# Kernel optimization log

Measured on AMD Instinct MI355X. Metric: run time of the kernel, lower is better.

## Reference

```python
import jax, jax.numpy as jnp
import numpy as np

B, LQ, LK, D, H, DK, DV = 8, 1024, 1024, 512, 8, 64, 64
EPS = 1e-14          # K.epsilon()**2 with default K.epsilon()=1e-7
MASK_VALUE = -1e30   # default mask_value in call()


def setup_inputs() -> dict:
    key = jax.random.key(0)
    ks = jax.random.split(key, 7)
    query = jax.random.normal(ks[0], (B, LQ, D), jnp.float32)
    key_t = jax.random.normal(ks[1], (B, LK, D), jnp.float32)
    value = jax.random.normal(ks[2], (B, LK, D), jnp.float32)
    mask = jax.random.randint(ks[3], (B, LK), 0, 2).astype(jnp.float32)
    glorot = np.sqrt(2.0 / (D + DK)).astype(np.float32)
    Wq = jax.random.normal(ks[4], (H, D, DK), jnp.float32) * glorot
    Wk = jax.random.normal(ks[5], (H, D, DK), jnp.float32) * glorot
    Wv = jax.random.normal(ks[6], (H, D, DV), jnp.float32) * glorot
    gamma = jnp.ones((1,), jnp.float32)
    beta = jnp.zeros((1,), jnp.float32)
    return {"query": query, "key": key_t, "value": value, "mask": mask,
            "Wq": Wq, "Wk": Wk, "Wv": Wv, "gamma": gamma, "beta": beta}


def reference(query, key, value, mask, Wq, Wk, Wv, gamma, beta):
    # Per-head projections (the original's Python loop over heads, vectorized).
    q = jnp.einsum('bqd,hde->bhqe', query, Wq)   # [B,H,LQ,DK]
    k = jnp.einsum('bkd,hde->bhke', key, Wk)     # [B,H,LK,DK]
    v = jnp.einsum('bkd,hde->bhke', value, Wv)   # [B,H,LK,DV]
    # NOTE: no 1/sqrt(dk) scaling, faithful to the source.
    A = jnp.einsum('bhqe,bhke->bhqk', q, k)      # [B,H,LQ,LK]
    m = mask[:, None, None, :]                    # [B,1,1,LK] broadcast over heads & queries
    A = m * A + (1.0 - m) * MASK_VALUE
    A = jax.nn.softmax(A, axis=-1)
    o = jnp.einsum('bhqk,bhke->bhqe', A, v)      # [B,H,LQ,DV]
    conc = o.transpose(0, 2, 1, 3).reshape(B, LQ, H * DV)  # concat heads
    # Scalar-affine layernorm over the concatenated feature dim.
    mean = jnp.mean(conc, axis=-1, keepdims=True)
    var = jnp.mean(jnp.square(conc - mean), axis=-1, keepdims=True)
    x = (conc - mean) / jnp.sqrt(var + EPS)
    return x * gamma[0] + beta[0]
```

## Files before the change

### kernel.cpp

```cpp
#include <hip/hip_runtime.h>
#include <math.h>

#define NB 8
#define NLQ 1024
#define NLK 1024
#define ND 512
#define NH 8
#define MASKV -1e30f
#define LOG2E 1.44269504088896f
#define SHIFT2 32.0f

typedef unsigned short ushort_t;
typedef __attribute__((ext_vector_type(8))) _Float16 f16x8;
typedef __attribute__((ext_vector_type(8))) short bf16x8;
typedef __attribute__((ext_vector_type(16))) float f32x16;

__device__ __forceinline__ ushort_t f2h_bits(float f) {
    union { _Float16 h; ushort_t u; } v; v.h = (_Float16)f;
    return v.u;
}
__device__ __forceinline__ ushort_t f2bf(float f) {
    union { float f; unsigned u; } v; v.f = f;
    unsigned r = v.u + 0x7fffu + ((v.u >> 16) & 1u);
    return (ushort_t)(r >> 16);
}
__device__ __forceinline__ void gload16(const ushort_t* g, ushort_t* l) {
    __builtin_amdgcn_global_load_lds(
        (const __attribute__((address_space(1))) void*)g,
        (__attribute__((address_space(3))) void*)l, 16, 0, 0);
}
__device__ __forceinline__ unsigned pack_bf16_trunc(float p0, float p1) {
    return __builtin_amdgcn_perm(__float_as_uint(p1), __float_as_uint(p0),
                                 0x07060302u);
}

__global__ __launch_bounds__(256) void wsplit_kernel(
    const float* __restrict__ Wq, const float* __restrict__ Wk, const float* __restrict__ Wv,
    ushort_t* __restrict__ oq, ushort_t* __restrict__ ok, ushort_t* __restrict__ ov) {
    __shared__ float T[64][65];
    const int d0 = blockIdx.x * 64;
    const int h  = blockIdx.y;
    const int t  = blockIdx.z;
    const float* W = (t == 0) ? Wq : (t == 1) ? Wk : Wv;
    ushort_t* oh = (t == 0) ? oq : (t == 1) ? ok : ov;
    const int tid = threadIdx.x;
#pragma unroll
    for (int i = 0; i < 4; i++) {
        int r = (tid >> 4) + i * 16;
        int c = (tid & 15) * 4;
        float4 v = *(const float4*)&W[((size_t)h * ND + d0 + r) * 64 + c];
        *(float4*)&T[r][c] = v;
    }
    __syncthreads();
    const int e = tid & 63;
    const int dg = tid >> 6;
    ushort_t hs[16];
#pragma unroll
    for (int dd = 0; dd < 16; dd++) hs[dd] = f2h_bits(T[dg * 16 + dd][e]);
    size_t base = ((size_t)h * 64 + e) * ND + d0 + dg * 16;
#pragma unroll
    for (int c = 0; c < 2; c++) {
        uint4 wh;
        wh.x = (unsigned)hs[8*c+0] | ((unsigned)hs[8*c+1] << 16);
        wh.y = (unsigned)hs[8*c+2] | ((unsigned)hs[8*c+3] << 16);
        wh.z = (unsigned)hs[8*c+4] | ((unsigned)hs[8*c+5] << 16);
        wh.w = (unsigned)hs[8*c+6] | ((unsigned)hs[8*c+7] << 16);
        *(uint4*)&oh[base + 8 * c] = wh;
    }
}

__global__ __launch_bounds__(256, 2) void proj_gemm_kernel(
    const float* __restrict__ Xq, const float* __restrict__ Xk,
    const float* __restrict__ Xv, const ushort_t* __restrict__ Wbase,
    ushort_t* __restrict__ Obase) {
    __shared__ ushort_t sA[2][8320];
    __shared__ ushort_t sB[2][8320];

    const int bid   = blockIdx.x;
    const int y     = bid / 192;
    const int mglob = bid % 192;
    const int t  = mglob >> 6;
    const int b  = (mglob >> 3) & 7;
    const int l0 = (mglob & 7) * 128;

    const int tid  = threadIdx.x;
    const int wave = tid >> 6;
    const int lane = tid & 63;
    const int l31  = lane & 31;
    const int hib  = lane >> 5;
    const int wr = wave >> 1, wc = wave & 1;

    const float* Xt = (t == 0) ? Xq : (t == 1) ? Xk : Xv;
    const float* gx = Xt + ((size_t)b * NLQ + l0) * ND;
    const ushort_t* gwt = Wbase + (size_t)t * ((size_t)NH * 64 * ND)
                        + (size_t)y * 128 * ND;
    ushort_t* out = Obase + (size_t)t * ((size_t)NB * NH * NLQ * 64);

    const int srow = lane >> 3;
    const int schk = (lane & 7) ^ srow;

    float4 ax[4][2];
    auto aload = [&](int d0) {
#pragma unroll
        for (int j = 0; j < 4; j++) {
            int row = (j * 4 + wave) * 8 + srow;
            const float* p = gx + (size_t)row * ND + d0 + schk * 8;
            ax[j][0] = *(const float4*)p;
            ax[j][1] = *(const float4*)(p + 4);
        }
    };
    auto awrite = [&](int buf) {
#pragma unroll
        for (int j = 0; j < 4; j++) {
            int u = j * 4 + wave;
            uint4 hv;
            hv.x = (unsigned)f2h_bits(ax[j][0].x) | ((unsigned)f2h_bits(ax[j][0].y) << 16);
            hv.y = (unsigned)f2h_bits(ax[j][0].z) | ((unsigned)f2h_bits(ax[j][0].w) << 16);
            hv.z = (unsigned)f2h_bits(ax[j][1].x) | ((unsigned)f2h_bits(ax[j][1].y) << 16);
            hv.w = (unsigned)f2h_bits(ax[j][1].z) | ((unsigned)f2h_bits(ax[j][1].w) << 16);
            *(uint4*)(sA[buf] + u * 520 + lane * 8) = hv;
        }
    };
    auto bstage = [&](int buf, int d0) {
#pragma unroll
        for (int j = 0; j < 4; j++) {
            int u = j * 4 + wave;
            int row = u * 8 + srow;
            gload16(gwt + (size_t)row * ND + d0 + schk * 8, sB[buf] + u * 520);
        }
    };

    f32x16 acc00, acc01, acc10, acc11;
#pragma unroll
    for (int i = 0; i < 16; i++) { acc00[i] = 0.f; acc01[i] = 0.f;
                                   acc10[i] = 0.f; acc11[i] = 0.f; }

    const int ga  = wr * 8 + (l31 >> 3);
    const int gb  = wc * 8 + (l31 >> 3);
    const int ro  = (l31 & 7) * 64;
    const int swz = l31 & 7;

    auto mfma_chunk = [&](int buf) {
#pragma unroll
        for (int c = 0; c < 4; c++) {
            const int pc = ((2 * c + hib) ^ swz) * 8;
            f16x8 a0 = *(const f16x8*)&sA[buf][ga * 520 + ro + pc];
            f16x8 a1 = *(const f16x8*)&sA[buf][(ga + 4) * 520 + ro + pc];
            f16x8 b0 = *(const f16x8*)&sB[buf][gb * 520 + ro + pc];
            f16x8 b1 = *(const f16x8*)&sB[buf][(gb + 4) * 520 + ro + pc];
            acc00 = __builtin_amdgcn_mfma_f32_32x32x16_f16(a0, b0, acc00, 0, 0, 0);
            acc01 = __builtin_amdgcn_mfma_f32_32x32x16_f16(a0, b1, acc01, 0, 0, 0);
            acc10 = __builtin_amdgcn_mfma_f32_32x32x16_f16(a1, b0, acc10, 0, 0, 0);
            acc11 = __builtin_amdgcn_mfma_f32_32x32x16_f16(a1, b1, acc11, 0, 0, 0);
        }
    };

    aload(0);
    bstage(0, 0);
    asm volatile("s_waitcnt vmcnt(4)" ::: "memory");
    __builtin_amdgcn_sched_barrier(0);
    awrite(0);
    aload(64);
    asm volatile("s_waitcnt vmcnt(8)" ::: "memory");
    asm volatile("s_waitcnt lgkmcnt(0)" ::: "memory");
    __builtin_amdgcn_sched_barrier(0);
    __builtin_amdgcn_s_barrier();

    int cur = 0;
#pragma unroll
    for (int kc = 0; kc < 8; kc++) {
        if (kc < 7) {
            bstage(cur ^ 1, (kc + 1) * 64);
            mfma_chunk(cur);
            asm volatile("s_waitcnt vmcnt(4)" ::: "memory");
            __builtin_amdgcn_sched_barrier(0);
            awrite(cur ^ 1);
            if (kc < 6) {
                aload((kc + 2) * 64);
                asm volatile("s_waitcnt vmcnt(8)" ::: "memory");
            } else {
                asm volatile("s_waitcnt vmcnt(0)" ::: "memory");
            }
            asm volatile("s_waitcnt lgkmcnt(0)" ::: "memory");
            __builtin_amdgcn_sched_barrier(0);
            __builtin_amdgcn_s_barrier();
        } else {
            mfma_chunk(cur);
        }
        cur ^= 1;
    }

    if (t < 2) {
        const float scale = (t == 0) ? LOG2E : 1.f;
#pragma unroll
        for (int mi = 0; mi < 2; mi++) {
#pragma unroll
            for (int ni = 0; ni < 2; ni++) {
                const f32x16& a = (mi == 0) ? (ni == 0 ? acc00 : acc01)
                                            : (ni == 0 ? acc10 : acc11);
                int nglob = y * 128 + wc * 64 + ni * 32 + l31;
                int hh = nglob >> 6, e = nglob & 63;
                size_t obase = (((size_t)b * NH + hh) * NLQ + l0) * 64 + e;
#pragma unroll
                for (int r = 0; r < 16; r++) {
                    int l = wr * 64 + mi * 32 + (r & 3) + 8 * (r >> 2) + 4 * hib;
                    out[obase + (size_t)l * 64] = f2h_bits(a[r] * scale);
                }
            }
        }
    } else {
        __syncthreads();
        ushort_t (*T)[130] = (ushort_t(*)[130])sA;
#pragma unroll
        for (int mi = 0; mi < 2; mi++) {
#pragma unroll
            for (int ni = 0; ni < 2; ni++) {
                const f32x16& a = (mi == 0) ? (ni == 0 ? acc00 : acc01)
                                            : (ni == 0 ? acc10 : acc11);
                int n_loc = wc * 64 + ni * 32 + l31;
#pragma unroll
                for (int r = 0; r < 16; r++) {
                    int l = wr * 64 + mi * 32 + (r & 3) + 8 * (r >> 2) + 4 * hib;
                    T[n_loc][l] = f2bf(a[r]);
                }
            }
        }
        __syncthreads();
        const int n_loc = tid >> 1;
        const int half  = tid & 1;
        const int hh = n_loc >> 6, e = n_loc & 63;
        size_t obase = (((size_t)b * NH + y * 2 + hh) * 64 + e) * NLK
                     + l0 + half * 64;
        const ushort_t* src = &T[n_loc][half * 64];
#pragma unroll
        for (int c2 = 0; c2 < 8; c2++)
            *(uint4*)&out[obase + c2 * 8] = *(const uint4*)&src[c2 * 8];
    }
}

__global__ __launch_bounds__(256, 4) void attn_kernel(
    const ushort_t* __restrict__ Qf, const ushort_t* __restrict__ Kf,
    const ushort_t* __restrict__ Vt, const float* __restrict__ maskp,
    float* __restrict__ Op) {
    __shared__ ushort_t sK[2][4160];
    __shared__ ushort_t sV[2][4160];
    __shared__ float sBias[1024];

    const int idx = blockIdx.x;
    const int bh_i = idx & 63;
    const int qc  = idx >> 6;
    const int b = bh_i >> 3, h = bh_i & 7;
    const size_t bh = (size_t)b * NH + h;

    const int tid  = threadIdx.x;
    const int wave = tid >> 6;
    const int lane = tid & 63;
    const int l31  = lane & 31;
    const int hib  = lane >> 5;
    const int q = qc * 128 + wave * 32 + l31;
    const int sw = l31 & 7;

    {
        const float* mrow = maskp + ((size_t)b << 10);
        float4 m0 = *(const float4*)&mrow[tid * 4];
        float4 bi;
        bi.x = (m0.x > 0.5f) ? -SHIFT2 : MASKV;
        bi.y = (m0.y > 0.5f) ? -SHIFT2 : MASKV;
        bi.z = (m0.z > 0.5f) ? -SHIFT2 : MASKV;
        bi.w = (m0.w > 0.5f) ? -SHIFT2 : MASKV;
        *(float4*)&sBias[tid * 4] = bi;
    }

    f16x8 qh[4];
    {
        const ushort_t* ph = Qf + (bh * NLQ + q) * 64 + hib * 8;
#pragma unroll
        for (int c = 0; c < 4; c++) qh[c] = *(const f16x8*)(ph + c * 16);
    }

    const int srow = lane >> 3;
    const int schk = (lane & 7) ^ srow;

    auto stage = [&](int buf, int k0) {
#pragma unroll
        for (int n = 0; n < 4; n++) {
            int u = wave + n * 4;
            if (u < 8) {
                int row = u * 8 + srow;
                int key = (row & ~12) | ((row & 4) << 1) | ((row & 8) >> 1);
                gload16(Kf + ((bh << 10) + k0 + key) * 64 + schk * 8,
                        sK[buf] + u * 520);
            } else {
                int u8 = u - 8;
                int row = u8 * 8 + srow;
                gload16(Vt + ((bh << 6) + row) * NLK + k0 + schk * 8,
                        sV[buf] + u8 * 520);
            }
        }
    };

    f32x16 O0, O1;
#pragma unroll
    for (int i = 0; i < 16; i++) { O0[i] = 0.f; O1[i] = 0.f; }
    float lrun = 0.f;

    const int rp0 = (l31 >> 3) * 520 + (l31 & 7) * 64;
    const int rp1 = rp0 + 4 * 520;

    stage(0, 0);
    __syncthreads();
    int cur = 0;

    for (int t = 0; t < 16; t++) {
        const int k0 = t << 6;
        if (t < 15) stage(cur ^ 1, k0 + 64);

        f32x16 S0, S1;
#pragma unroll
        for (int g = 0; g < 4; g++) {
            const int kb = k0 + 16 * (g >> 1) + 8 * hib + 4 * (g & 1);
            float4 b0 = *(const float4*)&sBias[kb];
            float4 b1 = *(const float4*)&sBias[kb + 32];
            S0[4 * g + 0] = b0.x; S0[4 * g + 1] = b0.y;
            S0[4 * g + 2] = b0.z; S0[4 * g + 3] = b0.w;
            S1[4 * g + 0] = b1.x; S1[4 * g + 1] = b1.y;
            S1[4 * g + 2] = b1.z; S1[4 * g + 3] = b1.w;
        }
#pragma unroll
        for (int c = 0; c < 4; c++) {
            const int pc = ((2 * c + hib) ^ sw) * 8;
            f16x8 a0 = *(const f16x8*)&sK[cur][rp0 + pc];
            f16x8 a1 = *(const f16x8*)&sK[cur][rp1 + pc];
            S0 = __builtin_amdgcn_mfma_f32_32x32x16_f16(a0, qh[c], S0, 0, 0, 0);
            S1 = __builtin_amdgcn_mfma_f32_32x32x16_f16(a1, qh[c], S1, 0, 0, 0);
        }

        unsigned pq[8][2];
#pragma unroll
        for (int g = 0; g < 8; g++) {
            float p0, p1, p2, p3;
            if (g < 4) {
                p0 = __builtin_amdgcn_exp2f(S0[4*g+0]);
                p1 = __builtin_amdgcn_exp2f(S0[4*g+1]);
                p2 = __builtin_amdgcn_exp2f(S0[4*g+2]);
                p3 = __builtin_amdgcn_exp2f(S0[4*g+3]);
            } else {
                p0 = __builtin_amdgcn_exp2f(S1[4*(g-4)+0]);
                p1 = __builtin_amdgcn_exp2f(S1[4*(g-4)+1]);
                p2 = __builtin_amdgcn_exp2f(S1[4*(g-4)+2]);
                p3 = __builtin_amdgcn_exp2f(S1[4*(g-4)+3]);
            }
            lrun += (p0 + p1) + (p2 + p3);
            pq[g][0] = pack_bf16_trunc(p0, p1);
            pq[g][1] = pack_bf16_trunc(p2, p3);
        }

#pragma unroll
        for (int c = 0; c < 4; c++) {
            union { unsigned u[4]; bf16x8 v; } pf;
            pf.u[0] = pq[2 * c][0];     pf.u[1] = pq[2 * c][1];
            pf.u[2] = pq[2 * c + 1][0]; pf.u[3] = pq[2 * c + 1][1];
            const int pc = ((2 * c + hib) ^ sw) * 8;
            bf16x8 v0 = *(const bf16x8*)&sV[cur][rp0 + pc];
            bf16x8 v1 = *(const bf16x8*)&sV[cur][rp1 + pc];
            O0 = __builtin_amdgcn_mfma_f32_32x32x16_bf16(v0, pf.v, O0, 0, 0, 0);
            O1 = __builtin_amdgcn_mfma_f32_32x32x16_bf16(v1, pf.v, O1, 0, 0, 0);
        }
        __syncthreads();
        cur ^= 1;
    }

    lrun += __shfl_xor(lrun, 32);
    const float linv = 1.f / lrun;
    float* obase = Op + ((size_t)(b * NLQ + q)) * (NH * 64) + h * 64;
#pragma unroll
    for (int me = 0; me < 2; me++) {
#pragma unroll
        for (int g = 0; g < 4; g++) {
            int e0 = me * 32 + 8 * g + 4 * hib;
            float4 o;
            if (me == 0) {
                o.x = O0[4 * g + 0] * linv; o.y = O0[4 * g + 1] * linv;
                o.z = O0[4 * g + 2] * linv; o.w = O0[4 * g + 3] * linv;
            } else {
                o.x = O1[4 * g + 0] * linv; o.y = O1[4 * g + 1] * linv;
                o.z = O1[4 * g + 2] * linv; o.w = O1[4 * g + 3] * linv;
            }
            *(float4*)&obase[e0] = o;
        }
    }
}

__global__ __launch_bounds__(256) void ln_kernel(const float* __restrict__ X,
                                                 const float* __restrict__ gamma,
                                                 const float* __restrict__ beta,
                                                 float* __restrict__ out) {
    const int row = blockIdx.x * 4 + (threadIdx.x >> 6);
    const int lane = threadIdx.x & 63;
    const float* x = &X[(size_t)row * 512];
    float4 v0 = *(const float4*)&x[lane * 8];
    float4 v1 = *(const float4*)&x[lane * 8 + 4];
    float sum = v0.x + v0.y + v0.z + v0.w + v1.x + v1.y + v1.z + v1.w;
    float sq = v0.x * v0.x + v0.y * v0.y + v0.z * v0.z + v0.w * v0.w
             + v1.x * v1.x + v1.y * v1.y + v1.z * v1.z + v1.w * v1.w;
#pragma unroll
    for (int off = 32; off > 0; off >>= 1) {
        sum += __shfl_down(sum, off);
        sq  += __shfl_down(sq, off);
    }
    sum = __shfl(sum, 0);
    sq  = __shfl(sq, 0);
    const float mean = sum * (1.f / 512.f);
    const float var = sq * (1.f / 512.f) - mean * mean;
    const float rstd = rsqrtf(var + 1e-14f);
    const float g = gamma[0], be = beta[0];
    float* o = &out[(size_t)row * 512];
    float4 r0, r1;
    r0.x = (v0.x - mean) * rstd * g + be;  r0.y = (v0.y - mean) * rstd * g + be;
    r0.z = (v0.z - mean) * rstd * g + be;  r0.w = (v0.w - mean) * rstd * g + be;
    r1.x = (v1.x - mean) * rstd * g + be;  r1.y = (v1.y - mean) * rstd * g + be;
    r1.z = (v1.z - mean) * rstd * g + be;  r1.w = (v1.w - mean) * rstd * g + be;
    *(float4*)&o[lane * 8] = r0;
    *(float4*)&o[lane * 8 + 4] = r1;
}

extern "C" void kernel_launch(void* const* d_in, const int* in_sizes, int n_in,
                              void* d_out, int out_size, void* d_ws, size_t ws_size,
                              hipStream_t stream) {
    const float* query = (const float*)d_in[0];
    const float* key_t = (const float*)d_in[1];
    const float* value = (const float*)d_in[2];
    const float* mask  = (const float*)d_in[3];
    const float* Wq    = (const float*)d_in[4];
    const float* Wk    = (const float*)d_in[5];
    const float* Wv    = (const float*)d_in[6];
    const float* gamma = (const float*)d_in[7];
    const float* beta  = (const float*)d_in[8];
    float* out = (float*)d_out;

    const size_t A = (size_t)NB * NLQ * ND;
    const size_t WS = (size_t)NH * 64 * ND;
    ushort_t* Qf = (ushort_t*)d_ws;
    ushort_t* Kf = Qf + A;
    ushort_t* Vt = Qf + 2 * A;
    ushort_t* Wt = Qf + 3 * A;

    wsplit_kernel<<<dim3(ND / 64, NH, 3), 256, 0, stream>>>(
        Wq, Wk, Wv, Wt, Wt + WS, Wt + 2 * WS);

    proj_gemm_kernel<<<768, 256, 0, stream>>>(
        query, key_t, value, Wt, Qf);

    attn_kernel<<<512, 256, 0, stream>>>(Qf, Kf, Vt, mask, out);

    ln_kernel<<<(NB * NLQ) / 4, 256, 0, stream>>>(out, gamma, beta, out);
}
```

Measured before the change: 165.4 us.

## Load projection weight fragments directly from global memory instead of via LDS

```diff
diff --git a/kernel.cpp b/kernel.cpp
--- a/kernel.cpp
+++ b/kernel.cpp
@@ -69,12 +69,11 @@
     }
 }
 
-__global__ __launch_bounds__(256, 2) void proj_gemm_kernel(
+__global__ __launch_bounds__(256, 3) void proj_gemm_kernel(
     const float* __restrict__ Xq, const float* __restrict__ Xk,
     const float* __restrict__ Xv, const ushort_t* __restrict__ Wbase,
     ushort_t* __restrict__ Obase) {
     __shared__ ushort_t sA[2][8320];
-    __shared__ ushort_t sB[2][8320];
 
     const int bid   = blockIdx.x;
     const int y     = bid / 192;
@@ -121,14 +120,6 @@
             *(uint4*)(sA[buf] + u * 520 + lane * 8) = hv;
         }
     };
-    auto bstage = [&](int buf, int d0) {
-#pragma unroll
-        for (int j = 0; j < 4; j++) {
-            int u = j * 4 + wave;
-            int row = u * 8 + srow;
-            gload16(gwt + (size_t)row * ND + d0 + schk * 8, sB[buf] + u * 520);
-        }
-    };
 
     f32x16 acc00, acc01, acc10, acc11;
 #pragma unroll
@@ -136,57 +127,39 @@
                                    acc10[i] = 0.f; acc11[i] = 0.f; }
 
     const int ga  = wr * 8 + (l31 >> 3);
-    const int gb  = wc * 8 + (l31 >> 3);
     const int ro  = (l31 & 7) * 64;
     const int swz = l31 & 7;
 
-    auto mfma_chunk = [&](int buf) {
+    const ushort_t* gb0 = gwt
+        + (size_t)(wc * 64 + (l31 >> 3) * 8 + (l31 & 7)) * ND;
+
+    aload(0);
+    awrite(0);
+    __syncthreads();
+
+    int cur = 0;
+#pragma unroll
+    for (int kc = 0; kc < 8; kc++) {
+        if (kc < 7) aload((kc + 1) * 64);
+        f16x8 bfr[2][4];
+#pragma unroll
+        for (int ni = 0; ni < 2; ni++)
+#pragma unroll
+            for (int c = 0; c < 4; c++)
+                bfr[ni][c] = *(const f16x8*)&gb0[(size_t)ni * 32 * ND
+                                                 + kc * 64 + (2 * c + hib) * 8];
 #pragma unroll
         for (int c = 0; c < 4; c++) {
             const int pc = ((2 * c + hib) ^ swz) * 8;
-            f16x8 a0 = *(const f16x8*)&sA[buf][ga * 520 + ro + pc];
-            f16x8 a1 = *(const f16x8*)&sA[buf][(ga + 4) * 520 + ro + pc];
-            f16x8 b0 = *(const f16x8*)&sB[buf][gb * 520 + ro + pc];
-            f16x8 b1 = *(const f16x8*)&sB[buf][(gb + 4) * 520 + ro + pc];
-            acc00 = __builtin_amdgcn_mfma_f32_32x32x16_f16(a0, b0, acc00, 0, 0, 0);
-            acc01 = __builtin_amdgcn_mfma_f32_32x32x16_f16(a0, b1, acc01, 0, 0, 0);
-            acc10 = __builtin_amdgcn_mfma_f32_32x32x16_f16(a1, b0, acc10, 0, 0, 0);
-            acc11 = __builtin_amdgcn_mfma_f32_32x32x16_f16(a1, b1, acc11, 0, 0, 0);
-        }
-    };
-
-    aload(0);
-    bstage(0, 0);
-    asm volatile("s_waitcnt vmcnt(4)" ::: "memory");
-    __builtin_amdgcn_sched_barrier(0);
-    awrite(0);
-    aload(64);
-    asm volatile("s_waitcnt vmcnt(8)" ::: "memory");
-    asm volatile("s_waitcnt lgkmcnt(0)" ::: "memory");
-    __builtin_amdgcn_sched_barrier(0);
-    __builtin_amdgcn_s_barrier();
-
-    int cur = 0;
-#pragma unroll
-    for (int kc = 0; kc < 8; kc++) {
-        if (kc < 7) {
-            bstage(cur ^ 1, (kc + 1) * 64);
-            mfma_chunk(cur);
-            asm volatile("s_waitcnt vmcnt(4)" ::: "memory");
-            __builtin_amdgcn_sched_barrier(0);
-            awrite(cur ^ 1);
-            if (kc < 6) {
-                aload((kc + 2) * 64);
-                asm volatile("s_waitcnt vmcnt(8)" ::: "memory");
-            } else {
-                asm volatile("s_waitcnt vmcnt(0)" ::: "memory");
-            }
-            asm volatile("s_waitcnt lgkmcnt(0)" ::: "memory");
-            __builtin_amdgcn_sched_barrier(0);
-            __builtin_amdgcn_s_barrier();
-        } else {
-            mfma_chunk(cur);
-        }
+            f16x8 a0 = *(const f16x8*)&sA[cur][ga * 520 + ro + pc];
+            f16x8 a1 = *(const f16x8*)&sA[cur][(ga + 4) * 520 + ro + pc];
+            acc00 = __builtin_amdgcn_mfma_f32_32x32x16_f16(a0, bfr[0][c], acc00, 0, 0, 0);
+            acc01 = __builtin_amdgcn_mfma_f32_32x32x16_f16(a0, bfr[1][c], acc01, 0, 0, 0);
+            acc10 = __builtin_amdgcn_mfma_f32_32x32x16_f16(a1, bfr[0][c], acc10, 0, 0, 0);
+            acc11 = __builtin_amdgcn_mfma_f32_32x32x16_f16(a1, bfr[1][c], acc11, 0, 0, 0);
+        }
+        if (kc < 7) awrite(cur ^ 1);
+        __syncthreads();
         cur ^= 1;
     }
 
```

Result: slower. 173.5 us (+4.9%).
